# Kernel optimization log

Hardware: AMD Instinct MI355X
Metric: run time of the kernel (lower is better)

Reference implementation:

```python
import jax, jax.numpy as jnp
import numpy as np

EPS = 1e-5

def _act_quant(x, bits=8):
    # per-token absmax quantization to signed int range, dequantized (STE)
    qb = float(2 ** (bits - 1) - 1)  # 127 for 8 bits
    scale = qb / jnp.clip(jnp.max(jnp.abs(x), axis=-1, keepdims=True), EPS, None)
    x_dq = jnp.clip(jnp.round(x * scale), -qb, qb) / scale
    return x + jax.lax.stop_gradient(x_dq - x)

def _weight_quant(w):
    # BitNet b1.58 ternary weights: scale = mean |W|, values in {-1,0,1} * scale (STE)
    s = jnp.clip(jnp.mean(jnp.abs(w)), EPS, None)
    w_dq = jnp.clip(jnp.round(w / s), -1.0, 1.0) * s
    return w + jax.lax.stop_gradient(w_dq - w)

def _bitlinear(x, w, bits=8):
    # x: [..., in], w: [out, in]
    return jnp.einsum('bsi,oi->bso', _act_quant(x, bits), _weight_quant(w))

def setup_inputs() -> dict:
    key = jax.random.key(0)
    k1, k2, k3 = jax.random.split(key, 3)
    B, S, H = 4, 4096, 2048
    I = int(H * 2.0)
    return {
        'hidden_states': jax.random.normal(k1, (B, S, H), dtype=jnp.float32),
        'w_up': jax.random.normal(k2, (I, H), dtype=jnp.float32) * (1.0 / np.sqrt(H)),
        'w_down': jax.random.normal(k3, (H, I), dtype=jnp.float32) * (1.0 / np.sqrt(I)),
    }

def reference(hidden_states, w_up, w_down):
    bits = 8
    h = _bitlinear(hidden_states, w_up, bits)          # [B,S,I]
    h = jnp.square(jax.nn.relu(h))                      # squared ReLU
    # dropout p=0.0 (eval) -> identity
    out = _bitlinear(h, w_down, bits)                   # [B,S,H]
    return out
```

## Files before the change

kernel.cpp:

```cpp
#include <hip/hip_runtime.h>
#include <hip/hip_bf16.h>

typedef signed char i8_t;
typedef _Float16 half_t;
typedef float v4fl __attribute__((ext_vector_type(4)));
typedef _Float16 v8h __attribute__((ext_vector_type(8)));
typedef int v4i __attribute__((ext_vector_type(4)));
typedef signed char v8c __attribute__((ext_vector_type(8)));
typedef signed char v16c __attribute__((ext_vector_type(16)));

__device__ __forceinline__ float ternqf(float w, float s) {
    float q = rintf(w / s);
    return fminf(1.f, fmaxf(-1.f, q));
}

__device__ __forceinline__ void gload16(const void* g, void* l) {
    __builtin_amdgcn_global_load_lds(
        (const __attribute__((address_space(1))) void*)g,
        (__attribute__((address_space(3))) void*)l, 16, 0, 0);
}

__global__ void abssum_partial2(const float* __restrict__ wup,
                                const float* __restrict__ wdn, long n,
                                float* __restrict__ part_up,
                                float* __restrict__ part_dn) {
    const int half = gridDim.x >> 1;
    const bool up = (blockIdx.x < half);
    const float* w = up ? wup : wdn;
    float* partial = up ? part_up : part_dn;
    const int bid = up ? blockIdx.x : blockIdx.x - half;
    long i0 = ((long)bid * 256 + threadIdx.x) * 8;
    long stride = (long)half * 256 * 8;
    float s = 0.f;
    for (long i = i0; i < n; i += stride) {
        v4fl a = *(const v4fl*)(w + i);
        v4fl b = *(const v4fl*)(w + i + 4);
#pragma unroll
        for (int j = 0; j < 4; ++j) s += fabsf(a[j]) + fabsf(b[j]);
    }
#pragma unroll
    for (int off = 32; off > 0; off >>= 1) s += __shfl_down(s, off, 64);
    __shared__ __align__(16) float red[4];
    if ((threadIdx.x & 63) == 0) red[threadIdx.x >> 6] = s;
    __syncthreads();
    if (threadIdx.x == 0)
        partial[bid] = (red[0] + red[1]) + (red[2] + red[3]);
}

__global__ void abssum_final(const float* __restrict__ part_up,
                             const float* __restrict__ part_dn,
                             float* __restrict__ scales, float inv) {
    const int wv = threadIdx.x >> 6;
    const int l = threadIdx.x & 63;
    const float* part = wv ? part_dn : part_up;
    float s = ((part[l] + part[l + 64]) + (part[l + 128] + part[l + 192]));
#pragma unroll
    for (int off = 32; off > 0; off >>= 1) s += __shfl_down(s, off, 64);
    if (l == 0) scales[wv] = fmaxf(s * inv, 1e-5f);
}

__global__ void wquant2_kernel(const float* __restrict__ wup,
                               const float* __restrict__ wdn,
                               i8_t* __restrict__ wqu, i8_t* __restrict__ wqd,
                               const float* __restrict__ scales, int wblocks) {
    const bool up = ((int)blockIdx.x < wblocks);
    const float* w = up ? wup : wdn;
    i8_t* wq = up ? wqu : wqd;
    const float s = up ? scales[0] : scales[1];
    const int bid = up ? blockIdx.x : blockIdx.x - wblocks;
    long i = ((long)bid * 256 + threadIdx.x) * 8;
    v4fl a = *(const v4fl*)(w + i);
    v4fl b = *(const v4fl*)(w + i + 4);
    v8c o;
#pragma unroll
    for (int j = 0; j < 4; ++j) {
        o[j]     = (i8_t)(int)ternqf(a[j], s);
        o[j + 4] = (i8_t)(int)ternqf(b[j], s);
    }
    *(v8c*)(wq + i) = o;
}

template <int W>
__global__ void rowquant_kernel(const float* __restrict__ src, i8_t* __restrict__ dst,
                                float* __restrict__ scale_out, int rows) {
    const int l = threadIdx.x & 63;
    const int row = blockIdx.x * 4 + (threadIdx.x >> 6);
    if (row >= rows) return;
    const int NI = W / 1024;
    const float* p = src + (size_t)row * W + l * 16;
    float v[NI * 16];
#pragma unroll
    for (int it = 0; it < NI; ++it) {
#pragma unroll
        for (int c = 0; c < 4; ++c) {
            v4fl a = *(const v4fl*)(p + it * 1024 + c * 4);
#pragma unroll
            for (int e = 0; e < 4; ++e) v[it * 16 + c * 4 + e] = a[e];
        }
    }
    float amax = 0.f;
#pragma unroll
    for (int j = 0; j < NI * 16; ++j) amax = fmaxf(amax, fabsf(v[j]));
#pragma unroll
    for (int off = 32; off > 0; off >>= 1)
        amax = fmaxf(amax, __shfl_xor(amax, off, 64));
    const float m = fmaxf(amax, 1e-5f);
    if (l == 0) scale_out[row] = m / 127.f;
    const float sc = 127.f / m;
    i8_t* q = dst + (size_t)row * W + l * 16;
#pragma unroll
    for (int it = 0; it < NI; ++it) {
        v16c o;
#pragma unroll
        for (int j = 0; j < 16; ++j) {
            float t = rintf(v[it * 16 + j] * sc);
            o[j] = (i8_t)(int)fminf(127.f, fmaxf(-127.f, t));
        }
        *(v16c*)(q + it * 1024) = o;
    }
}

template <typename T, int NV>
__global__ void hamax_kernel(const T* __restrict__ h, float* __restrict__ scale_out,
                             float* __restrict__ recip_out) {
    const int row = blockIdx.x;
    const int tid = threadIdx.x;
    const T* p = h + (size_t)row * (NV * 2048);
    float amax = 0.f;
#pragma unroll
    for (int it = 0; it < NV; ++it) {
        const T* s = p + ((size_t)it * 256 + tid) * 8;
#pragma unroll
        for (int j = 0; j < 8; ++j) amax = fmaxf(amax, fabsf((float)s[j]));
    }
#pragma unroll
    for (int off = 32; off > 0; off >>= 1) amax = fmaxf(amax, __shfl_xor(amax, off, 64));
    __shared__ __align__(16) float red[4];
    if ((tid & 63) == 0) red[tid >> 6] = amax;
    __syncthreads();
    if (tid == 0) {
        float m = fmaxf(fmaxf(red[0], red[1]), fmaxf(red[2], red[3]));
        m = fmaxf(m, 1e-5f);
        scale_out[row] = m / 127.f;
        recip_out[row] = 127.f / m;
    }
}

__device__ __forceinline__ void stage_tile256(const i8_t* __restrict__ g, int K,
                                              i8_t* l, int tid) {
#pragma unroll
    for (int i = 0; i < 4; ++i) {
        const int c = i * 512 + tid;
        const int r = c >> 3;
        const int lc = (((c & 7) ^ (r & 7)) << 4);
        gload16(g + (size_t)r * K + lc, l + c * 16);
    }
}

#define MIDBAR() do { \
    __builtin_amdgcn_s_barrier(); \
    __builtin_amdgcn_sched_barrier(0); \
    asm volatile("s_waitcnt lgkmcnt(0)" ::: "memory"); \
    __builtin_amdgcn_sched_barrier(0); } while (0)

#define ENDBAR() do { \
    __builtin_amdgcn_sched_barrier(0); \
    __builtin_amdgcn_s_barrier(); \
    __builtin_amdgcn_sched_barrier(0); } while (0)

template <int EPI>
__launch_bounds__(512, 2)
__global__ void gemm_bt8(const i8_t* __restrict__ A, const i8_t* __restrict__ B,
                         void* __restrict__ Cv,
                         const float* __restrict__ rowscale,
                         const float* __restrict__ wscale,
                         int M, int N, int K) {
    __shared__ __align__(16) i8_t smem[131072];

    const int tid = threadIdx.x;

    const int gx = gridDim.x;
    const int nwg = gx * gridDim.y;
    int flat = blockIdx.y * gx + blockIdx.x;
    if ((nwg & 7) == 0) flat = (flat & 7) * (nwg >> 3) + (flat >> 3);
    const int n0 = (flat % gx) * 256;
    const int m0 = (flat / gx) * 256;

    const i8_t* gA = A + (size_t)m0 * K;
    const i8_t* gB = B + (size_t)n0 * K;

    const int w = tid >> 6, l = tid & 63;
    const int wr = w >> 2, wc = w & 3;
    const int lrow = l & 15, lq = l >> 4;
    const int lr7 = lrow & 7;
    const int kk0 = ((lq)     ^ lr7) << 4;
    const int kk1 = ((lq + 4) ^ lr7) << 4;
    const int aBase = ((wr * 128 + lrow) << 7);
    const int bBase = ((wc * 64 + lrow) << 7);

    v4i acc[8][4];
#pragma unroll
    for (int a = 0; a < 8; ++a)
#pragma unroll
        for (int b = 0; b < 4; ++b) acc[a][b] = (v4i){0, 0, 0, 0};

    const int NT = K >> 7;
    stage_tile256(gB, K, smem + 32768, tid);
    stage_tile256(gA, K, smem, tid);
    stage_tile256(gB + 128, K, smem + 65536 + 32768, tid);
    stage_tile256(gA + 128, K, smem + 65536, tid);
    asm volatile("s_waitcnt vmcnt(8)" ::: "memory");
    __builtin_amdgcn_s_barrier();
    __builtin_amdgcn_sched_barrier(0);

    for (int t = 0; t < NT; ++t) {
        i8_t* Ab = smem + ((t & 1) << 16);
        i8_t* Bb = Ab + 32768;
        const bool pf = (t + 2 < NT);

        v4i a0[4], a1[4], b0[4], b1[4];

#pragma unroll
        for (int mi = 0; mi < 4; ++mi)
            a0[mi] = *(const v4i*)(Ab + aBase + (mi << 11) + kk0);
#pragma unroll
        for (int nj = 0; nj < 4; ++nj)
            b0[nj] = *(const v4i*)(Bb + bBase + (nj << 11) + kk0);
        MIDBAR();
        __builtin_amdgcn_s_setprio(1);
#pragma unroll
        for (int mi = 0; mi < 4; ++mi)
#pragma unroll
            for (int nj = 0; nj < 4; ++nj)
                acc[mi][nj] = __builtin_amdgcn_mfma_i32_16x16x64_i8(
                    a0[mi], b0[nj], acc[mi][nj], 0, 0, 0);
        __builtin_amdgcn_s_setprio(0);
        ENDBAR();

#pragma unroll
        for (int mi = 0; mi < 4; ++mi)
            a1[mi] = *(const v4i*)(Ab + aBase + ((mi + 4) << 11) + kk0);
#pragma unroll
        for (int nj = 0; nj < 4; ++nj)
            b1[nj] = *(const v4i*)(Bb + bBase + (nj << 11) + kk1);
        MIDBAR();
        __builtin_amdgcn_s_setprio(1);
#pragma unroll
        for (int mi = 0; mi < 4; ++mi)
#pragma unroll
            for (int nj = 0; nj < 4; ++nj)
                acc[mi + 4][nj] = __builtin_amdgcn_mfma_i32_16x16x64_i8(
                    a1[mi], b0[nj], acc[mi + 4][nj], 0, 0, 0);
        __builtin_amdgcn_s_setprio(0);
        ENDBAR();

#pragma unroll
        for (int mi = 0; mi < 4; ++mi)
            a0[mi] = *(const v4i*)(Ab + aBase + (mi << 11) + kk1);
#pragma unroll
        for (int mi = 0; mi < 4; ++mi)
            a1[mi] = *(const v4i*)(Ab + aBase + ((mi + 4) << 11) + kk1);
        MIDBAR();
        __builtin_amdgcn_s_setprio(1);
#pragma unroll
        for (int mi = 0; mi < 4; ++mi)
#pragma unroll
            for (int nj = 0; nj < 4; ++nj)
                acc[mi][nj] = __builtin_amdgcn_mfma_i32_16x16x64_i8(
                    a0[mi], b1[nj], acc[mi][nj], 0, 0, 0);
        __builtin_amdgcn_s_setprio(0);
        ENDBAR();

        if (pf) {
            stage_tile256(gB + (size_t)(t + 2) * 128, K, Bb, tid);
            stage_tile256(gA + (size_t)(t + 2) * 128, K, Ab, tid);
        }
        MIDBAR();
        __builtin_amdgcn_s_setprio(1);
#pragma unroll
        for (int mi = 0; mi < 4; ++mi)
#pragma unroll
            for (int nj = 0; nj < 4; ++nj)
                acc[mi + 4][nj] = __builtin_amdgcn_mfma_i32_16x16x64_i8(
                    a1[mi], b1[nj], acc[mi + 4][nj], 0, 0, 0);
        __builtin_amdgcn_s_setprio(0);
        __builtin_amdgcn_sched_barrier(0);
        if (pf) {
            asm volatile("s_waitcnt vmcnt(8)" ::: "memory");
        } else if (t + 1 < NT) {
            asm volatile("s_waitcnt vmcnt(0)" ::: "memory");
        }
        if (t + 1 < NT) {
            __builtin_amdgcn_s_barrier();
            __builtin_amdgcn_sched_barrier(0);
        }
    }

    const float sw = wscale[0];
#pragma unroll
    for (int mi = 0; mi < 8; ++mi) {
#pragma unroll
        for (int r = 0; r < 4; ++r) {
            const int row = m0 + wr * 128 + mi * 16 + lq * 4 + r;
            const float rs = sw * rowscale[row];
#pragma unroll
            for (int nj = 0; nj < 4; ++nj) {
                const int col = n0 + wc * 64 + nj * 16 + lrow;
                float v = (float)acc[mi][nj][r] * rs;
                if (EPI == 0) {
                    ((float*)Cv)[(size_t)row * N + col] = v;
                } else {
                    v = fmaxf(v, 0.f); v = v * v;
                    ((float*)Cv)[(size_t)row * N + col] = v;
                }
            }
        }
    }
}

template <int ASRC, int EPI>
__launch_bounds__(256, 2)
__global__ void gemm_bt(const void* __restrict__ Av, const i8_t* __restrict__ B,
                        void* __restrict__ Cv,
                        const float* __restrict__ rowscale,
                        const float* __restrict__ arecip,
                        const float* __restrict__ wscale,
                        int M, int N, int K) {
    __shared__ __align__(16) i8_t As[128 * 64];
    __shared__ __align__(16) i8_t Bs[128 * 64];

    const int tid = threadIdx.x;
    const int gx = gridDim.x;
    const int nwg = gx * gridDim.y;
    int flat = blockIdx.y * gx + blockIdx.x;
    if ((nwg & 7) == 0) flat = (flat & 7) * (nwg >> 3) + (flat >> 3);
    const int n0 = (flat % gx) * 128;
    const int m0 = (flat / gx) * 128;

    const int srow = tid >> 2;
    const int scol = (tid & 3) * 16;
    const i8_t* gB0 = B + (size_t)(n0 + srow) * K + scol;
    const i8_t* gB1 = B + (size_t)(n0 + 64 + srow) * K + scol;
    i8_t* lB0 = Bs + tid * 16;
    i8_t* lB1 = Bs + 4096 + tid * 16;

    const i8_t* gA0 = nullptr;
    const i8_t* gA1 = nullptr;
    i8_t* lA0 = As + tid * 16;
    i8_t* lA1 = As + 4096 + tid * 16;
    if (ASRC == 0) {
        gA0 = (const i8_t*)Av + (size_t)(m0 + srow) * K + scol;
        gA1 = (const i8_t*)Av + (size_t)(m0 + 64 + srow) * K + scol;
    }

    const int qrow = tid >> 1;
    const int qcol = (tid & 1) * 32;
    const float* gA32 = (const float*)Av + (size_t)(m0 + qrow) * K + qcol;
    const half_t* gAh = (const half_t*)Av + (size_t)(m0 + qrow) * K + qcol;
    i8_t* qdst = As + qrow * 64 + qcol;
    const float qsc = (ASRC != 0) ? arecip[m0 + qrow] : 0.f;

    const int w = tid >> 6, l = tid & 63;
    const int wr = w >> 1, wc = w & 1;
    const int lrow = l & 15, lq = l >> 4;

    v4i acc[4][4];
#pragma unroll
    for (int a = 0; a < 4; ++a)
#pragma unroll
        for (int b = 0; b < 4; ++b) acc[a][b] = (v4i){0, 0, 0, 0};

    const int kiters = K / 64;
    for (int kt = 0; kt < kiters; ++kt) {
        const int off = kt * 64;
        v16c r0, r1;
        if (ASRC == 1) {
#pragma unroll
            for (int c = 0; c < 4; ++c) {
                v4fl f0 = *(const v4fl*)(gA32 + off + c * 4);
                v4fl f1 = *(const v4fl*)(gA32 + off + 16 + c * 4);
#pragma unroll
                for (int e = 0; e < 4; ++e) {
                    float t0 = rintf(f0[e] * qsc);
                    float t1 = rintf(f1[e] * qsc);
                    r0[c * 4 + e] = (i8_t)(int)fminf(127.f, fmaxf(-127.f, t0));
                    r1[c * 4 + e] = (i8_t)(int)fminf(127.f, fmaxf(-127.f, t1));
                }
            }
        } else if (ASRC == 2) {
#pragma unroll
            for (int c = 0; c < 2; ++c) {
                v8h h0 = *(const v8h*)(gAh + off + c * 8);
                v8h h1 = *(const v8h*)(gAh + off + 16 + c * 8);
#pragma unroll
                for (int e = 0; e < 8; ++e) {
                    float t0 = rintf((float)h0[e] * qsc);
                    float t1 = rintf((float)h1[e] * qsc);
                    r0[c * 8 + e] = (i8_t)(int)fminf(127.f, fmaxf(-127.f, t0));
                    r1[c * 8 + e] = (i8_t)(int)fminf(127.f, fmaxf(-127.f, t1));
                }
            }
        }
        __syncthreads();
        gload16(gB0 + off, lB0);
        gload16(gB1 + off, lB1);
        if (ASRC == 0) {
            gload16(gA0 + off, lA0);
            gload16(gA1 + off, lA1);
        } else {
            *(v16c*)qdst = r0;
            *(v16c*)(qdst + 16) = r1;
        }
        __syncthreads();

        v4i af[4], bfr[4];
#pragma unroll
        for (int mi = 0; mi < 4; ++mi)
            af[mi] = *(const v4i*)(As + (wr * 64 + mi * 16 + lrow) * 64 + lq * 16);
#pragma unroll
        for (int nj = 0; nj < 4; ++nj)
            bfr[nj] = *(const v4i*)(Bs + (wc * 64 + nj * 16 + lrow) * 64 + lq * 16);
#pragma unroll
        for (int mi = 0; mi < 4; ++mi)
#pragma unroll
            for (int nj = 0; nj < 4; ++nj)
                acc[mi][nj] = __builtin_amdgcn_mfma_i32_16x16x64_i8(
                    af[mi], bfr[nj], acc[mi][nj], 0, 0, 0);
    }

    const float sw = wscale[0];
#pragma unroll
    for (int mi = 0; mi < 4; ++mi) {
#pragma unroll
        for (int r = 0; r < 4; ++r) {
            const int row = m0 + wr * 64 + mi * 16 + lq * 4 + r;
            const float rs = sw * rowscale[row];
#pragma unroll
            for (int nj = 0; nj < 4; ++nj) {
                const int col = n0 + wc * 64 + nj * 16 + lrow;
                float v = (float)acc[mi][nj][r] * rs;
                if (EPI == 0) {
                    ((float*)Cv)[(size_t)row * N + col] = v;
                } else if (EPI == 1) {
                    v = fmaxf(v, 0.f); v = v * v;
                    ((half_t*)Cv)[(size_t)row * N + col] = (half_t)v;
                } else {
                    v = fmaxf(v, 0.f); v = v * v;
                    ((float*)Cv)[(size_t)row * N + col] = v;
                }
            }
        }
    }
}

extern "C" void kernel_launch(void* const* d_in, const int* in_sizes, int n_in,
                              void* d_out, int out_size, void* d_ws, size_t ws_size,
                              hipStream_t stream) {
    const float* x   = (const float*)d_in[0];
    const float* wup = (const float*)d_in[1];
    const float* wdn = (const float*)d_in[2];

    const int H = 2048;
    const int T = in_sizes[0] / H;
    const int I = in_sizes[1] / H;
    const long nw = (long)in_sizes[1];
    const float winv = 1.0f / (float)nw;

    char* p = (char*)d_ws;
    float* scales  = (float*)p;
    float* part_up = (float*)(p + 256);
    float* part_dn = (float*)(p + 1280);
    float* a_scale = (float*)(p + 2304);
    float* h_scale = a_scale + T;
    float* h_recip = h_scale + T;
    size_t off = 2304 + (size_t)12 * T;
    off = (off + 255) & ~(size_t)255;
    i8_t* xq  = (i8_t*)(p + off); off += (size_t)T * H;
    off = (off + 255) & ~(size_t)255;
    i8_t* wqu = (i8_t*)(p + off); off += (size_t)I * H;
    off = (off + 255) & ~(size_t)255;
    i8_t* wqd = (i8_t*)(p + off); off += (size_t)H * I;
    off = (off + 255) & ~(size_t)255;
    void* h  = (void*)(p + off);
    i8_t* hq = (i8_t*)(p + off + (size_t)T * I * 4);

    const size_t need_full = off + (size_t)T * I * 5;
    const size_t need_h32  = off + (size_t)T * I * 4;
    const int mode = (ws_size == 0 || need_full <= ws_size) ? 0
                   : (need_h32 <= ws_size ? 1 : 2);
    const bool big_ok = (T % 256 == 0) && (I % 256 == 0) && (H % 256 == 0) &&
                        (H >= 256) && (I >= 256);

    abssum_partial2<<<512, 256, 0, stream>>>(wup, wdn, nw, part_up, part_dn);
    abssum_final<<<1, 128, 0, stream>>>(part_up, part_dn, scales, winv);

    int wblocks = (int)(nw / 2048);
    wquant2_kernel<<<2 * wblocks, 256, 0, stream>>>(wup, wdn, wqu, wqd, scales, wblocks);

    rowquant_kernel<2048><<<(T + 3) / 4, 256, 0, stream>>>(x, xq, a_scale, T);

    if (mode == 0 && big_ok) {
        gemm_bt8<2><<<dim3(I / 256, T / 256), 512, 0, stream>>>(
            xq, wqu, h, a_scale, scales + 0, T, I, H);
        rowquant_kernel<4096><<<(T + 3) / 4, 256, 0, stream>>>(
            (const float*)h, hq, h_scale, T);
        gemm_bt8<0><<<dim3(H / 256, T / 256), 512, 0, stream>>>(
            hq, wqd, d_out, h_scale, scales + 1, T, H, I);
    } else if (mode == 0) {
        gemm_bt<0, 2><<<dim3(I / 128, T / 128), 256, 0, stream>>>(
            xq, wqu, h, a_scale, nullptr, scales + 0, T, I, H);
        rowquant_kernel<4096><<<(T + 3) / 4, 256, 0, stream>>>(
            (const float*)h, hq, h_scale, T);
        gemm_bt<0, 0><<<dim3(H / 128, T / 128), 256, 0, stream>>>(
            hq, wqd, d_out, h_scale, nullptr, scales + 1, T, H, I);
    } else if (mode == 1) {
        gemm_bt<0, 2><<<dim3(I / 128, T / 128), 256, 0, stream>>>(
            xq, wqu, h, a_scale, nullptr, scales + 0, T, I, H);
        hamax_kernel<float, 2><<<T, 256, 0, stream>>>((const float*)h, h_scale, h_recip);
        gemm_bt<1, 0><<<dim3(H / 128, T / 128), 256, 0, stream>>>(
            h, wqd, d_out, h_scale, h_recip, scales + 1, T, H, I);
    } else {
        gemm_bt<0, 1><<<dim3(I / 128, T / 128), 256, 0, stream>>>(
            xq, wqu, h, a_scale, nullptr, scales + 0, T, I, H);
        hamax_kernel<half_t, 2><<<T, 256, 0, stream>>>((const half_t*)h, h_scale, h_recip);
        gemm_bt<2, 0><<<dim3(H / 128, T / 128), 256, 0, stream>>>(
            h, wqd, d_out, h_scale, h_recip, scales + 1, T, H, I);
    }
}
```

Before: 644.3 us.

## Remove per-phase barriers in int8 GEMM loop and software-pipeline LDS reads

Replaces the barrier-plus-full-lgkmcnt wait around each of the four MFMA phases with partial lgkmcnt waits, so LDS fragment loads for the next phase are issued while the current phase's MFMAs run. Only one workgroup barrier remains before the global-to-LDS prefetch overwrites the buffer, plus the end-of-iteration one. This cuts synchronization stalls and exposes LDS latency overlap. It relies on the hand-counted lgkmcnt values matching the issued ds_reads, and it may raise register pressure by keeping more fragments live.

```diff
diff --git a/kernel.cpp b/kernel.cpp
--- a/kernel.cpp
+++ b/kernel.cpp
@@ -157,16 +157,7 @@
     }
 }
 
-#define MIDBAR() do { \
-    __builtin_amdgcn_s_barrier(); \
-    __builtin_amdgcn_sched_barrier(0); \
-    asm volatile("s_waitcnt lgkmcnt(0)" ::: "memory"); \
-    __builtin_amdgcn_sched_barrier(0); } while (0)
-
-#define ENDBAR() do { \
-    __builtin_amdgcn_sched_barrier(0); \
-    __builtin_amdgcn_s_barrier(); \
-    __builtin_amdgcn_sched_barrier(0); } while (0)
+#define SB() __builtin_amdgcn_sched_barrier(0)
 
 template <int EPI>
 __launch_bounds__(512, 2)
@@ -211,7 +202,7 @@
     stage_tile256(gA + 128, K, smem + 65536, tid);
     asm volatile("s_waitcnt vmcnt(8)" ::: "memory");
     __builtin_amdgcn_s_barrier();
-    __builtin_amdgcn_sched_barrier(0);
+    SB();
 
     for (int t = 0; t < NT; ++t) {
         i8_t* Ab = smem + ((t & 1) << 16);
@@ -221,12 +212,21 @@
         v4i a0[4], a1[4], b0[4], b1[4];
 
 #pragma unroll
-        for (int mi = 0; mi < 4; ++mi)
-            a0[mi] = *(const v4i*)(Ab + aBase + (mi << 11) + kk0);
-#pragma unroll
         for (int nj = 0; nj < 4; ++nj)
             b0[nj] = *(const v4i*)(Bb + bBase + (nj << 11) + kk0);
-        MIDBAR();
+#pragma unroll
+        for (int mi = 0; mi < 4; ++mi)
+            a0[mi] = *(const v4i*)(Ab + aBase + (mi << 11) + kk0);
+        SB();
+#pragma unroll
+        for (int nj = 0; nj < 4; ++nj)
+            b1[nj] = *(const v4i*)(Bb + bBase + (nj << 11) + kk1);
+#pragma unroll
+        for (int mi = 0; mi < 4; ++mi)
+            a1[mi] = *(const v4i*)(Ab + aBase + ((mi + 4) << 11) + kk0);
+        SB();
+        asm volatile("s_waitcnt lgkmcnt(8)" ::: "memory");
+        SB();
         __builtin_amdgcn_s_setprio(1);
 #pragma unroll
         for (int mi = 0; mi < 4; ++mi)
@@ -235,15 +235,13 @@
                 acc[mi][nj] = __builtin_amdgcn_mfma_i32_16x16x64_i8(
                     a0[mi], b0[nj], acc[mi][nj], 0, 0, 0);
         __builtin_amdgcn_s_setprio(0);
-        ENDBAR();
-
-#pragma unroll
-        for (int mi = 0; mi < 4; ++mi)
-            a1[mi] = *(const v4i*)(Ab + aBase + ((mi + 4) << 11) + kk0);
-#pragma unroll
-        for (int nj = 0; nj < 4; ++nj)
-            b1[nj] = *(const v4i*)(Bb + bBase + (nj << 11) + kk1);
-        MIDBAR();
+        SB();
+#pragma unroll
+        for (int mi = 0; mi < 4; ++mi)
+            a0[mi] = *(const v4i*)(Ab + aBase + (mi << 11) + kk1);
+        SB();
+        asm volatile("s_waitcnt lgkmcnt(4)" ::: "memory");
+        SB();
         __builtin_amdgcn_s_setprio(1);
 #pragma unroll
         for (int mi = 0; mi < 4; ++mi)
@@ -252,15 +250,13 @@
                 acc[mi + 4][nj] = __builtin_amdgcn_mfma_i32_16x16x64_i8(
                     a1[mi], b0[nj], acc[mi + 4][nj], 0, 0, 0);
         __builtin_amdgcn_s_setprio(0);
-        ENDBAR();
-
-#pragma unroll
-        for (int mi = 0; mi < 4; ++mi)
-            a0[mi] = *(const v4i*)(Ab + aBase + (mi << 11) + kk1);
+        SB();
 #pragma unroll
         for (int mi = 0; mi < 4; ++mi)
             a1[mi] = *(const v4i*)(Ab + aBase + ((mi + 4) << 11) + kk1);
-        MIDBAR();
+        SB();
+        asm volatile("s_waitcnt lgkmcnt(4)" ::: "memory");
+        SB();
         __builtin_amdgcn_s_setprio(1);
 #pragma unroll
         for (int mi = 0; mi < 4; ++mi)
@@ -269,13 +265,16 @@
                 acc[mi][nj] = __builtin_amdgcn_mfma_i32_16x16x64_i8(
                     a0[mi], b1[nj], acc[mi][nj], 0, 0, 0);
         __builtin_amdgcn_s_setprio(0);
-        ENDBAR();
-
+        SB();
+        asm volatile("s_waitcnt lgkmcnt(0)" ::: "memory");
+        SB();
+        __builtin_amdgcn_s_barrier();
+        SB();
         if (pf) {
             stage_tile256(gB + (size_t)(t + 2) * 128, K, Bb, tid);
             stage_tile256(gA + (size_t)(t + 2) * 128, K, Ab, tid);
         }
-        MIDBAR();
+        SB();
         __builtin_amdgcn_s_setprio(1);
 #pragma unroll
         for (int mi = 0; mi < 4; ++mi)
@@ -284,7 +283,7 @@
                 acc[mi + 4][nj] = __builtin_amdgcn_mfma_i32_16x16x64_i8(
                     a1[mi], b1[nj], acc[mi + 4][nj], 0, 0, 0);
         __builtin_amdgcn_s_setprio(0);
-        __builtin_amdgcn_sched_barrier(0);
+        SB();
         if (pf) {
             asm volatile("s_waitcnt vmcnt(8)" ::: "memory");
         } else if (t + 1 < NT) {
@@ -292,7 +291,7 @@
         }
         if (t + 1 < NT) {
             __builtin_amdgcn_s_barrier();
-            __builtin_amdgcn_sched_barrier(0);
+            SB();
         }
     }
 
```

Result: faster. 619.4 us (-3.9%).
